# Optimization experiments

Measured on AMD Instinct MI355X. Metric: run time of the kernel, lower is better.

The kernel has to match this reference:

```python
import jax, jax.numpy as jnp
import numpy as np

B, H, S, DH = 2, 16, 2048, 64

def setup_inputs() -> dict:
    key = jax.random.key(0)
    k1, k2, k3 = jax.random.split(key, 3)
    return {
        "query": jax.random.normal(k1, (B, H, S, DH), dtype=jnp.float32),
        "key": jax.random.normal(k2, (B, H, S, DH), dtype=jnp.float32),
        "value": jax.random.normal(k3, (B, H, S, DH), dtype=jnp.float32),
        "key_padding_mask": jnp.zeros((B, S), dtype=bool),
    }

def reference(query, key, value, key_padding_mask):
    # scores: [B, H, Sq, Sk]
    scale = 1.0 / jnp.sqrt(jnp.asarray(query.shape[-1], query.dtype))
    scores = jnp.einsum("bhqd,bhkd->bhqk", query, key) * scale
    # key padding mask broadcasts over heads and query positions
    scores = jnp.where(key_padding_mask[:, None, None, :], -jnp.inf, scores)
    attn = jax.nn.softmax(scores, axis=-1)
    # dropout is identity in eval mode (deterministic reference)
    out = jnp.einsum("bhqk,bhkd->bhqd", attn, value)
    # [B, H, S, Dh] -> [B, S, H*Dh]
    b, h, s, dh = out.shape
    return out.transpose(0, 2, 1, 3).reshape(b, s, h * dh)
```

## Files before the change

kernel.cpp:

```cpp
#include <hip/hip_runtime.h>

typedef __attribute__((ext_vector_type(4))) float f32x4;
typedef __attribute__((ext_vector_type(4))) short s16x4;
typedef __attribute__((ext_vector_type(8))) short s16x8;

constexpr int Bn = 2, Hn = 16, Sn = 2048, DHn = 64;
constexpr int TQ = 64;
constexpr int TK = 64;
constexpr int NT = Sn / TK;
constexpr int LDK = 72;

__device__ __forceinline__ unsigned pk2(float a, float b) {
  unsigned ua = __builtin_bit_cast(unsigned, a);
  unsigned ub = __builtin_bit_cast(unsigned, b);
  ua += 0x7fffu + ((ua >> 16) & 1u);
  ub += 0x7fffu + ((ub >> 16) & 1u);
  return (ua >> 16) | (ub & 0xffff0000u);
}

__device__ __forceinline__ float fexp2(float x) {
#if __has_builtin(__builtin_amdgcn_exp2f)
  return __builtin_amdgcn_exp2f(x);
#else
  return exp2f(x);
#endif
}

__global__ __launch_bounds__(256, 4)
void fattn_kernel(const float* __restrict__ Qg, const float* __restrict__ Kg,
                  const float* __restrict__ Vg, const unsigned char* __restrict__ maskg,
                  float* __restrict__ Og) {
  __shared__ __align__(16) short Ksh[TK * LDK];
  __shared__ __align__(16) short VTsh[DHn * LDK];
  __shared__ __align__(16) short Psh[4 * 16 * LDK];
  __shared__ __align__(16) float Mb[TK];

  const int tid  = threadIdx.x;
  const int w    = tid >> 6;
  const int lane = tid & 63;
  const int n    = lane & 15;
  const int q4   = lane >> 4;

  const int blk = blockIdx.x;
  const int bh  = blk & 31;
  const int qt  = blk >> 5;
  const int b   = bh >> 4;
  const int h   = bh & 15;

  const float* Qb = Qg + (size_t)bh * Sn * DHn;
  const float* Kb = Kg + (size_t)bh * Sn * DHn;
  const float* Vb = Vg + (size_t)bh * Sn * DHn;
  const unsigned char* mbp = maskg + (size_t)b * Sn;

  const int q0 = qt * TQ + w * 16;

  const float c1 = 0.125f * 1.4426950408889634f;
  s16x8 qf[2];
  {
    const float* qrow = Qb + (size_t)(q0 + n) * DHn;
#pragma unroll
    for (int kc = 0; kc < 2; ++kc) {
      const float4* p = (const float4*)(qrow + kc * 32 + q4 * 8);
      float4 x = p[0], y = p[1];
      union { unsigned u[4]; s16x8 v; } tmp;
      tmp.u[0] = pk2(x.x * c1, x.y * c1);
      tmp.u[1] = pk2(x.z * c1, x.w * c1);
      tmp.u[2] = pk2(y.x * c1, y.y * c1);
      tmp.u[3] = pk2(y.z * c1, y.w * c1);
      qf[kc] = tmp.v;
    }
  }

  f32x4 Oa[4];
#pragma unroll
  for (int na = 0; na < 4; ++na) Oa[na] = (f32x4){0.f, 0.f, 0.f, 0.f};
  float m2   = -1e30f;
  float lsum = 0.f;

  for (int t = 0; t < NT; ++t) {
    __syncthreads();

#pragma unroll
    for (int i = 0; i < 4; ++i) {
      int linear = i * 256 + tid;
      int row = linear >> 4, c4 = linear & 15;
      float4 v = *(const float4*)(Kb + (size_t)(t * TK + row) * DHn + c4 * 4);
      union { unsigned u[2]; s16x4 v4; } st;
      st.u[0] = pk2(v.x, v.y);
      st.u[1] = pk2(v.z, v.w);
      *(s16x4*)&Ksh[row * LDK + c4 * 4] = st.v4;
    }
    {
      int tx = tid & 15, ty = tid >> 4;
      int r0 = ty * 4, c0 = tx * 4;
      float4 r_[4];
#pragma unroll
      for (int i = 0; i < 4; ++i)
        r_[i] = *(const float4*)(Vb + (size_t)(t * TK + r0 + i) * DHn + c0);
      float c_[4][4] = {
          {r_[0].x, r_[1].x, r_[2].x, r_[3].x},
          {r_[0].y, r_[1].y, r_[2].y, r_[3].y},
          {r_[0].z, r_[1].z, r_[2].z, r_[3].z},
          {r_[0].w, r_[1].w, r_[2].w, r_[3].w}};
      const int chunk = ((ty >> 1) ^ (tx & 7));
      const int half  = ty & 1;
#pragma unroll
      for (int j = 0; j < 4; ++j) {
        union { unsigned u[2]; s16x4 v4; } st;
        st.u[0] = pk2(c_[j][0], c_[j][1]);
        st.u[1] = pk2(c_[j][2], c_[j][3]);
        *(s16x4*)&VTsh[(c0 + j) * LDK + chunk * 8 + half * 4] = st.v4;
      }
    }
    if (tid < TK) Mb[tid] = mbp[t * TK + tid] ? -1e30f : 0.0f;
    __syncthreads();

    s16x8 kf[4][2];
#pragma unroll
    for (int mc = 0; mc < 4; ++mc)
#pragma unroll
      for (int kc = 0; kc < 2; ++kc)
        kf[mc][kc] = *(const s16x8*)&Ksh[(mc * 16 + n) * LDK + kc * 32 + q4 * 8];

    f32x4 sa[4];
#pragma unroll
    for (int mc = 0; mc < 4; ++mc)
      sa[mc] = *(const f32x4*)&Mb[mc * 16 + q4 * 4];
#pragma unroll
    for (int mc = 0; mc < 4; ++mc)
#pragma unroll
      for (int kc = 0; kc < 2; ++kc)
        sa[mc] = __builtin_amdgcn_mfma_f32_16x16x32_bf16(kf[mc][kc], qf[kc], sa[mc], 0, 0, 0);

    float tm = -3.0e38f;
#pragma unroll
    for (int mc = 0; mc < 4; ++mc)
#pragma unroll
      for (int r = 0; r < 4; ++r) tm = fmaxf(tm, sa[mc][r]);
    tm = fmaxf(tm, __shfl_xor(tm, 16));
    tm = fmaxf(tm, __shfl_xor(tm, 32));
    float mn    = fmaxf(m2, tm);
    float alpha = fexp2(m2 - mn);
    m2 = mn;

    float ls = 0.f;
#pragma unroll
    for (int mc = 0; mc < 4; ++mc) {
      float p0 = fexp2(sa[mc][0] - mn);
      float p1 = fexp2(sa[mc][1] - mn);
      float p2 = fexp2(sa[mc][2] - mn);
      float p3 = fexp2(sa[mc][3] - mn);
      ls += (p0 + p1) + (p2 + p3);
      union { unsigned u[2]; s16x4 v4; } pw;
      pw.u[0] = pk2(p0, p1);
      pw.u[1] = pk2(p2, p3);
      *(s16x4*)&Psh[(w * 16 + n) * LDK + mc * 16 + q4 * 4] = pw.v4;
    }
    ls += __shfl_xor(ls, 16);
    ls += __shfl_xor(ls, 32);
    lsum = lsum * alpha + ls;

#pragma unroll
    for (int r = 0; r < 4; ++r) {
      float ar = __shfl(alpha, q4 * 4 + r);
#pragma unroll
      for (int na = 0; na < 4; ++na) Oa[na][r] *= ar;
    }

    s16x8 vf[4][2];
#pragma unroll
    for (int na = 0; na < 4; ++na) {
#pragma unroll
      for (int kc = 0; kc < 2; ++kc) {
        int d = na * 16 + n;
        int chunk = (kc * 4 + q4) ^ ((4 * na + (n >> 2)) & 7);
        vf[na][kc] = *(const s16x8*)&VTsh[d * LDK + chunk * 8];
      }
    }
    s16x8 pf[2];
#pragma unroll
    for (int kc = 0; kc < 2; ++kc)
      pf[kc] = *(const s16x8*)&Psh[(w * 16 + n) * LDK + kc * 32 + q4 * 8];
#pragma unroll
    for (int na = 0; na < 4; ++na)
#pragma unroll
      for (int kc = 0; kc < 2; ++kc)
        Oa[na] = __builtin_amdgcn_mfma_f32_16x16x32_bf16(pf[kc], vf[na][kc], Oa[na], 0, 0, 0);
  }

#pragma unroll
  for (int r = 0; r < 4; ++r) {
    float lr  = __shfl(lsum, q4 * 4 + r);
    float inv = 1.0f / lr;
    int q = q0 + q4 * 4 + r;
    float* orow = Og + (size_t)(b * Sn + q) * (Hn * DHn) + h * DHn;
#pragma unroll
    for (int na = 0; na < 4; ++na)
      orow[na * 16 + n] = Oa[na][r] * inv;
  }
}

extern "C" void kernel_launch(void* const* d_in, const int* in_sizes, int n_in,
                              void* d_out, int out_size, void* d_ws, size_t ws_size,
                              hipStream_t stream) {
  (void)in_sizes; (void)n_in; (void)d_ws; (void)ws_size; (void)out_size;
  const float* Q = (const float*)d_in[0];
  const float* K = (const float*)d_in[1];
  const float* V = (const float*)d_in[2];
  const unsigned char* mask = (const unsigned char*)d_in[3];
  float* out = (float*)d_out;
  dim3 grid(Bn * Hn * (Sn / TQ));
  dim3 block(256);
  hipLaunchKernelGGL(fattn_kernel, grid, block, 0, stream, Q, K, V, mask, out);
}
```

Before: 176.7 us.

## Prepack K/V to swizzled bf16 tiles and stream them via global_load_lds

Adds a prepack kernel that converts K and V to bf16 once, with V transposed and both stored as XOR-swizzled 64x64 tiles in workspace. The attention kernel then copies each tile straight into LDS with global_load_lds instead of loading fp32, converting and transposing per block. This avoids repeating the conversion and transpose across the 32 query tiles and halves the bytes read per tile. The cost is an extra launch and an extra pass over K/V. Without a wait on the async LDS loads before the barrier, there is a risk of a race.

Result: faster. 166.6 us (-5.7%).

```diff
diff --git a/kernel.cpp b/kernel.cpp
--- a/kernel.cpp
+++ b/kernel.cpp
@@ -8,7 +8,7 @@
 constexpr int TQ = 64;
 constexpr int TK = 64;
 constexpr int NT = Sn / TK;
-constexpr int LDK = 72;
+constexpr int TILE_SH = TK * DHn;
 
 __device__ __forceinline__ unsigned pk2(float a, float b) {
   unsigned ua = __builtin_bit_cast(unsigned, a);
@@ -26,13 +26,61 @@
 #endif
 }
 
+__device__ __forceinline__ void gl2lds16(const short* g, short* l) {
+  __builtin_amdgcn_global_load_lds(
+      (const __attribute__((address_space(1))) void*)g,
+      (__attribute__((address_space(3))) void*)l, 16, 0, 0);
+}
+
 __global__ __launch_bounds__(256, 4)
-void fattn_kernel(const float* __restrict__ Qg, const float* __restrict__ Kg,
-                  const float* __restrict__ Vg, const unsigned char* __restrict__ maskg,
+void prepack_kernel(const float* __restrict__ Kg, const float* __restrict__ Vg,
+                    short* __restrict__ Kp, short* __restrict__ Vp) {
+  const int blk = blockIdx.x;
+  const int tid = threadIdx.x;
+  const float* Kt = Kg + (size_t)blk * TILE_SH;
+  const float* Vt = Vg + (size_t)blk * TILE_SH;
+  short* Kd = Kp + (size_t)blk * TILE_SH;
+  short* Vd = Vp + (size_t)blk * TILE_SH;
+
+  {
+    const int r = tid >> 2;
+    const int cb = (tid & 3) * 2;
+#pragma unroll
+    for (int cc = 0; cc < 2; ++cc) {
+      int c = cb + cc;
+      const float4* p = (const float4*)(Kt + (size_t)r * DHn + c * 8);
+      float4 x = p[0], y = p[1];
+      union { unsigned u[4]; s16x8 v; } tmp;
+      tmp.u[0] = pk2(x.x, x.y); tmp.u[1] = pk2(x.z, x.w);
+      tmp.u[2] = pk2(y.x, y.y); tmp.u[3] = pk2(y.z, y.w);
+      *(s16x8*)&Kd[r * 64 + (c ^ (r & 7)) * 8] = tmp.v;
+    }
+  }
+  {
+    const int d = tid & 63;
+    const int kb = (tid >> 6) * 16;
+#pragma unroll
+    for (int cc = 0; cc < 2; ++cc) {
+      int k0 = kb + cc * 8;
+      float v0[8];
+#pragma unroll
+      for (int j = 0; j < 8; ++j) v0[j] = Vt[(size_t)(k0 + j) * DHn + d];
+      union { unsigned u[4]; s16x8 v; } tmp;
+      tmp.u[0] = pk2(v0[0], v0[1]); tmp.u[1] = pk2(v0[2], v0[3]);
+      tmp.u[2] = pk2(v0[4], v0[5]); tmp.u[3] = pk2(v0[6], v0[7]);
+      int c = k0 >> 3;
+      *(s16x8*)&Vd[d * 64 + (c ^ (d & 7)) * 8] = tmp.v;
+    }
+  }
+}
+
+__global__ __launch_bounds__(256, 4)
+void fattn_kernel(const float* __restrict__ Qg, const short* __restrict__ Kp,
+                  const short* __restrict__ Vp, const unsigned char* __restrict__ maskg,
                   float* __restrict__ Og) {
-  __shared__ __align__(16) short Ksh[TK * LDK];
-  __shared__ __align__(16) short VTsh[DHn * LDK];
-  __shared__ __align__(16) short Psh[4 * 16 * LDK];
+  __shared__ __align__(16) short Ksh[TILE_SH];
+  __shared__ __align__(16) short VTsh[TILE_SH];
+  __shared__ __align__(16) short Psh[4 * 16 * 64];
   __shared__ __align__(16) float Mb[TK];
 
   const int tid  = threadIdx.x;
@@ -40,6 +88,7 @@
   const int lane = tid & 63;
   const int n    = lane & 15;
   const int q4   = lane >> 4;
+  const int swz  = n & 7;
 
   const int blk = blockIdx.x;
   const int bh  = blk & 31;
@@ -48,9 +97,9 @@
   const int h   = bh & 15;
 
   const float* Qb = Qg + (size_t)bh * Sn * DHn;
-  const float* Kb = Kg + (size_t)bh * Sn * DHn;
-  const float* Vb = Vg + (size_t)bh * Sn * DHn;
-  const unsigned char* mbp = maskg + (size_t)b * Sn;
+  const short* Kt = Kp + (size_t)bh * NT * TILE_SH;
+  const short* Vt = Vp + (size_t)bh * NT * TILE_SH;
+  const unsigned char* mq = maskg + (size_t)b * Sn;
 
   const int q0 = qt * TQ + w * 16;
 
@@ -71,57 +120,36 @@
     }
   }
 
+  const int c0   = q4 ^ swz;
+  const int offA = n * 64 + c0 * 8;
+  const int offB = n * 64 + (c0 ^ 4) * 8;
+  const int prow = (w * 16 + n) * 64;
+  const int pA   = prow + c0 * 8;
+  const int pB   = prow + (c0 ^ 4) * 8;
+  const int h01  = (q4 >> 1) ^ swz;
+  const int pwr  = prow + (q4 & 1) * 4;
+
   f32x4 Oa[4];
 #pragma unroll
   for (int na = 0; na < 4; ++na) Oa[na] = (f32x4){0.f, 0.f, 0.f, 0.f};
-  float m2   = -1e30f;
-  float lsum = 0.f;
+  float m2 = -1e30f, lsum = 0.f;
 
   for (int t = 0; t < NT; ++t) {
     __syncthreads();
 
-#pragma unroll
-    for (int i = 0; i < 4; ++i) {
-      int linear = i * 256 + tid;
-      int row = linear >> 4, c4 = linear & 15;
-      float4 v = *(const float4*)(Kb + (size_t)(t * TK + row) * DHn + c4 * 4);
-      union { unsigned u[2]; s16x4 v4; } st;
-      st.u[0] = pk2(v.x, v.y);
-      st.u[1] = pk2(v.z, v.w);
-      *(s16x4*)&Ksh[row * LDK + c4 * 4] = st.v4;
-    }
-    {
-      int tx = tid & 15, ty = tid >> 4;
-      int r0 = ty * 4, c0 = tx * 4;
-      float4 r_[4];
-#pragma unroll
-      for (int i = 0; i < 4; ++i)
-        r_[i] = *(const float4*)(Vb + (size_t)(t * TK + r0 + i) * DHn + c0);
-      float c_[4][4] = {
-          {r_[0].x, r_[1].x, r_[2].x, r_[3].x},
-          {r_[0].y, r_[1].y, r_[2].y, r_[3].y},
-          {r_[0].z, r_[1].z, r_[2].z, r_[3].z},
-          {r_[0].w, r_[1].w, r_[2].w, r_[3].w}};
-      const int chunk = ((ty >> 1) ^ (tx & 7));
-      const int half  = ty & 1;
-#pragma unroll
-      for (int j = 0; j < 4; ++j) {
-        union { unsigned u[2]; s16x4 v4; } st;
-        st.u[0] = pk2(c_[j][0], c_[j][1]);
-        st.u[1] = pk2(c_[j][2], c_[j][3]);
-        *(s16x4*)&VTsh[(c0 + j) * LDK + chunk * 8 + half * 4] = st.v4;
-      }
-    }
-    if (tid < TK) Mb[tid] = mbp[t * TK + tid] ? -1e30f : 0.0f;
+    gl2lds16(Kt + tid * 8,        &Ksh[w * 512]);
+    gl2lds16(Kt + 2048 + tid * 8, &Ksh[2048 + w * 512]);
+    gl2lds16(Vt + tid * 8,        &VTsh[w * 512]);
+    gl2lds16(Vt + 2048 + tid * 8, &VTsh[2048 + w * 512]);
+    if (tid < TK) Mb[tid] = mq[t * TK + tid] ? -1e30f : 0.0f;
     __syncthreads();
 
     s16x8 kf[4][2];
 #pragma unroll
-    for (int mc = 0; mc < 4; ++mc)
-#pragma unroll
-      for (int kc = 0; kc < 2; ++kc)
-        kf[mc][kc] = *(const s16x8*)&Ksh[(mc * 16 + n) * LDK + kc * 32 + q4 * 8];
-
+    for (int mc = 0; mc < 4; ++mc) {
+      kf[mc][0] = *(const s16x8*)&Ksh[mc * 1024 + offA];
+      kf[mc][1] = *(const s16x8*)&Ksh[mc * 1024 + offB];
+    }
     f32x4 sa[4];
 #pragma unroll
     for (int mc = 0; mc < 4; ++mc)
@@ -154,7 +182,7 @@
       union { unsigned u[2]; s16x4 v4; } pw;
       pw.u[0] = pk2(p0, p1);
       pw.u[1] = pk2(p2, p3);
-      *(s16x4*)&Psh[(w * 16 + n) * LDK + mc * 16 + q4 * 4] = pw.v4;
+      *(s16x4*)&Psh[pwr + ((h01 ^ (2 * mc)) * 8)] = pw.v4;
     }
     ls += __shfl_xor(ls, 16);
     ls += __shfl_xor(ls, 32);
@@ -170,22 +198,20 @@
     s16x8 vf[4][2];
 #pragma unroll
     for (int na = 0; na < 4; ++na) {
-#pragma unroll
-      for (int kc = 0; kc < 2; ++kc) {
-        int d = na * 16 + n;
-        int chunk = (kc * 4 + q4) ^ ((4 * na + (n >> 2)) & 7);
-        vf[na][kc] = *(const s16x8*)&VTsh[d * LDK + chunk * 8];
-      }
+      vf[na][0] = *(const s16x8*)&VTsh[na * 1024 + offA];
+      vf[na][1] = *(const s16x8*)&VTsh[na * 1024 + offB];
     }
     s16x8 pf[2];
-#pragma unroll
-    for (int kc = 0; kc < 2; ++kc)
-      pf[kc] = *(const s16x8*)&Psh[(w * 16 + n) * LDK + kc * 32 + q4 * 8];
+    pf[0] = *(const s16x8*)&Psh[pA];
+    pf[1] = *(const s16x8*)&Psh[pB];
 #pragma unroll
     for (int na = 0; na < 4; ++na)
 #pragma unroll
       for (int kc = 0; kc < 2; ++kc)
         Oa[na] = __builtin_amdgcn_mfma_f32_16x16x32_bf16(pf[kc], vf[na][kc], Oa[na], 0, 0, 0);
+
+    Kt += TILE_SH;
+    Vt += TILE_SH;
   }
 
 #pragma unroll
@@ -203,13 +229,17 @@
 extern "C" void kernel_launch(void* const* d_in, const int* in_sizes, int n_in,
                               void* d_out, int out_size, void* d_ws, size_t ws_size,
                               hipStream_t stream) {
-  (void)in_sizes; (void)n_in; (void)d_ws; (void)ws_size; (void)out_size;
+  (void)in_sizes; (void)n_in; (void)ws_size; (void)out_size;
   const float* Q = (const float*)d_in[0];
   const float* K = (const float*)d_in[1];
   const float* V = (const float*)d_in[2];
   const unsigned char* mask = (const unsigned char*)d_in[3];
   float* out = (float*)d_out;
-  dim3 grid(Bn * Hn * (Sn / TQ));
-  dim3 block(256);
-  hipLaunchKernelGGL(fattn_kernel, grid, block, 0, stream, Q, K, V, mask, out);
-}
+
+  short* Kp = (short*)d_ws;
+  short* Vp = Kp + (size_t)Bn * Hn * Sn * DHn;
+
+  hipLaunchKernelGGL(prepack_kernel, dim3(Bn * Hn * NT), dim3(256), 0, stream, K, V, Kp, Vp);
+  hipLaunchKernelGGL(fattn_kernel, dim3(Bn * Hn * (Sn / TQ)), dim3(256), 0, stream,
+                     Q, Kp, Vp, mask, out);
+}
```
